# Performance work log

Measured on AMD Instinct MI355X. Metric: run time of the kernel, lower is better.

Reference implementation:

```python
import jax, jax.numpy as jnp
import numpy as np

EPS = 1e-08
ATOM_CA = 1


def setup_inputs() -> dict:
    key = jax.random.key(0)
    k1, k2 = jax.random.split(key)
    B, N_RES, N_ATOMS = 256, 1024, 37
    pred_coords = jax.random.normal(k1, (B, N_RES, N_ATOMS, 3), dtype=jnp.float32)
    true_coords = jax.random.normal(k2, (B, N_RES, N_ATOMS, 3), dtype=jnp.float32)
    atom_mask = jnp.ones((B, N_RES, N_ATOMS), dtype=jnp.float32)
    return {"pred_coords": pred_coords, "true_coords": true_coords, "atom_mask": atom_mask}


def _kabsch_align(pred, true, mask):
    # pred/true: [B, N, 3], mask: [B, N]
    mask_sum = jnp.sum(mask, axis=1, keepdims=True) + EPS          # [B, 1]
    m = mask[..., None]                                             # [B, N, 1]
    pred_center = jnp.sum(pred * m, axis=1) / mask_sum              # [B, 3]
    true_center = jnp.sum(true * m, axis=1) / mask_sum              # [B, 3]
    pred_c = (pred - pred_center[:, None, :]) * m                   # [B, N, 3]
    true_c = (true - true_center[:, None, :]) * m                   # [B, N, 3]
    H = jnp.einsum('bni,bnj->bij', pred_c, true_c)                  # [B, 3, 3]
    U, s, Vh = jnp.linalg.svd(H)                                    # H = U diag(s) Vh
    V = jnp.swapaxes(Vh, -1, -2)
    Ut = jnp.swapaxes(U, -1, -2)
    det = jnp.linalg.det(jnp.matmul(V, Ut))                         # [B]
    sign = jnp.stack([jnp.ones_like(det), jnp.ones_like(det), det], axis=-1)  # [B, 3]
    S = jnp.eye(3, dtype=pred.dtype) * sign[:, None, :]             # diag(1,1,det)
    R = jnp.matmul(jnp.matmul(V, S), Ut)                            # [B, 3, 3]
    # aligned = (pred - pred_center) @ R^T + true_center
    aligned = jnp.einsum('bnj,bij->bni', pred - pred_center[:, None, :], R)
    return aligned + true_center[:, None, :]


def reference(pred_coords, true_coords, atom_mask):
    pred_ca = pred_coords[:, :, ATOM_CA, :]   # [B, N_res, 3]
    true_ca = true_coords[:, :, ATOM_CA, :]
    ca_mask = atom_mask[:, :, ATOM_CA]        # [B, N_res]
    pred_ca = _kabsch_align(pred_ca, true_ca, ca_mask)
    diff_sq = jnp.sum((pred_ca - true_ca) ** 2, axis=-1)            # [B, N_res]
    rmsd = jnp.sqrt(jnp.sum(diff_sq * ca_mask, axis=1) / (jnp.sum(ca_mask, axis=1) + EPS))
    return jnp.mean(rmsd)
```

## Files before the change

### kernel.cpp

```cpp
#include <hip/hip_runtime.h>
#include <math.h>

#define N_RES 1024
#define N_ATOMS 37
#define ATOM_CA 1
#define NBATCH 256
#define SLICES 4
#define NSUM 34

__global__ __launch_bounds__(256) void rmsd_moments_kernel(
    const float* __restrict__ pred, const float* __restrict__ truec,
    const float* __restrict__ mask, float* __restrict__ partials)
{
    const int blk   = blockIdx.x;
    const int b     = blk >> 2;
    const int slice = blk & 3;
    const int tid   = threadIdx.x;
    const int n     = slice * 256 + tid;

    const size_t resStride = (size_t)N_ATOMS * 3;
    const float* pp = pred  + ((size_t)b * N_RES + n) * resStride + ATOM_CA * 3;
    const float* tt = truec + ((size_t)b * N_RES + n) * resStride + ATOM_CA * 3;
    const float  m  = mask[((size_t)b * N_RES + n) * N_ATOMS + ATOM_CA];

    const float p0 = pp[0], p1 = pp[1], p2 = pp[2];
    const float t0 = tt[0], t1 = tt[1], t2 = tt[2];
    const float m2 = m * m;

    float acc[NSUM];
    acc[0] = m;
    acc[1] = m * p0;  acc[2] = m * p1;  acc[3] = m * p2;
    acc[4] = m * t0;  acc[5] = m * t1;  acc[6] = m * t2;
    acc[7] = m * (p0*p0 + p1*p1 + p2*p2);
    acc[8] = m * (t0*t0 + t1*t1 + t2*t2);
    acc[9]  = m * p0 * t0; acc[10] = m * p0 * t1; acc[11] = m * p0 * t2;
    acc[12] = m * p1 * t0; acc[13] = m * p1 * t1; acc[14] = m * p1 * t2;
    acc[15] = m * p2 * t0; acc[16] = m * p2 * t1; acc[17] = m * p2 * t2;
    acc[18] = m2;
    acc[19] = m2 * p0; acc[20] = m2 * p1; acc[21] = m2 * p2;
    acc[22] = m2 * t0; acc[23] = m2 * t1; acc[24] = m2 * t2;
    acc[25] = m2 * p0 * t0; acc[26] = m2 * p0 * t1; acc[27] = m2 * p0 * t2;
    acc[28] = m2 * p1 * t0; acc[29] = m2 * p1 * t1; acc[30] = m2 * p1 * t2;
    acc[31] = m2 * p2 * t0; acc[32] = m2 * p2 * t1; acc[33] = m2 * p2 * t2;

#pragma unroll
    for (int i = 0; i < NSUM; ++i) {
        float v = acc[i];
#pragma unroll
        for (int off = 32; off > 0; off >>= 1) v += __shfl_down(v, off, 64);
        acc[i] = v;
    }

    __shared__ float partial[4][NSUM];
    const int wave = tid >> 6, lane = tid & 63;
    if (lane == 0) {
#pragma unroll
        for (int i = 0; i < NSUM; ++i) partial[wave][i] = acc[i];
    }
    __syncthreads();
    if (tid < NSUM) {
        partials[(size_t)blk * NSUM + tid] =
            partial[0][tid] + partial[1][tid] + partial[2][tid] + partial[3][tid];
    }
}

__global__ __launch_bounds__(256) void rmsd_finish_kernel(
    const float* __restrict__ partials, float* __restrict__ out)
{
    const int b = threadIdx.x;

    double s[NSUM];
#pragma unroll
    for (int i = 0; i < NSUM; ++i) s[i] = 0.0;
#pragma unroll
    for (int k = 0; k < SLICES; ++k) {
        const float* row = partials + ((size_t)b * SLICES + k) * NSUM;
#pragma unroll
        for (int i = 0; i < NSUM; ++i) s[i] += (double)row[i];
    }

    const double M   = s[0];
    const double Mep = M + 1e-8;
    double Sp[3] = { s[1], s[2], s[3] };
    double St[3] = { s[4], s[5], s[6] };
    double pc[3] = { Sp[0] / Mep, Sp[1] / Mep, Sp[2] / Mep };
    double tc[3] = { St[0] / Mep, St[1] / Mep, St[2] / Mep };
    const double Qp = s[7], Qt = s[8];
    const double S2 = s[18];
    double S2p[3] = { s[19], s[20], s[21] };
    double S2t[3] = { s[22], s[23], s[24] };

    double H[3][3];
#pragma unroll
    for (int i = 0; i < 3; ++i)
#pragma unroll
        for (int j = 0; j < 3; ++j)
            H[i][j] = s[25 + i * 3 + j] - pc[i] * S2t[j] - tc[j] * S2p[i]
                    + pc[i] * tc[j] * S2;

    const float Sxx = (float)H[0][0], Sxy = (float)H[0][1], Sxz = (float)H[0][2];
    const float Syx = (float)H[1][0], Syy = (float)H[1][1], Syz = (float)H[1][2];
    const float Szx = (float)H[2][0], Szy = (float)H[2][1], Szz = (float)H[2][2];
    float A[4][4] = {
        { Sxx + Syy + Szz, Syz - Szy,        Szx - Sxz,        Sxy - Syx },
        { Syz - Szy,       Sxx - Syy - Szz,  Sxy + Syx,        Szx + Sxz },
        { Szx - Sxz,       Sxy + Syx,       -Sxx + Syy - Szz,  Syz + Szy },
        { Sxy - Syx,       Szx + Sxz,        Syz + Szy,       -Sxx - Syy + Szz }
    };
    float Vm[4][4] = { {1,0,0,0},{0,1,0,0},{0,0,1,0},{0,0,0,1} };

#pragma unroll
    for (int sweep = 0; sweep < 8; ++sweep) {
#pragma unroll
        for (int p = 0; p < 3; ++p) {
#pragma unroll
            for (int q = p + 1; q < 4; ++q) {
                const float apq = A[p][q];
                const float denom = fabsf(apq) > 1e-20f ? apq : 1e-20f;
                const float theta = (A[q][q] - A[p][p]) / (2.0f * denom);
                float tt = (theta >= 0.0f ? 1.0f : -1.0f)
                         / (fabsf(theta) + sqrtf(theta * theta + 1.0f));
                if (fabsf(apq) <= 1e-20f) tt = 0.0f;
                const float c = 1.0f / sqrtf(tt * tt + 1.0f);
                const float sn = tt * c;
#pragma unroll
                for (int k = 0; k < 4; ++k) {
                    const float akp = A[k][p], akq = A[k][q];
                    A[k][p] = c * akp - sn * akq;
                    A[k][q] = sn * akp + c * akq;
                }
#pragma unroll
                for (int k = 0; k < 4; ++k) {
                    const float apk = A[p][k], aqk = A[q][k];
                    A[p][k] = c * apk - sn * aqk;
                    A[q][k] = sn * apk + c * aqk;
                }
#pragma unroll
                for (int k = 0; k < 4; ++k) {
                    const float vkp = Vm[k][p], vkq = Vm[k][q];
                    Vm[k][p] = c * vkp - sn * vkq;
                    Vm[k][q] = sn * vkp + c * vkq;
                }
            }
        }
    }
    int best = 0;
#pragma unroll
    for (int i = 1; i < 4; ++i) if (A[i][i] > A[best][best]) best = i;
    float q0 = Vm[0][best], qx = Vm[1][best], qy = Vm[2][best], qz = Vm[3][best];
    const float nq = sqrtf(q0*q0 + qx*qx + qy*qy + qz*qz);
    q0 /= nq; qx /= nq; qy /= nq; qz /= nq;

    double R[3][3] = {
        { 1.0 - 2.0*((double)qy*qy + (double)qz*qz), 2.0*((double)qx*qy - (double)qz*q0), 2.0*((double)qx*qz + (double)qy*q0) },
        { 2.0*((double)qx*qy + (double)qz*q0), 1.0 - 2.0*((double)qx*qx + (double)qz*qz), 2.0*((double)qy*qz - (double)qx*q0) },
        { 2.0*((double)qx*qz - (double)qy*q0), 2.0*((double)qy*qz + (double)qx*q0), 1.0 - 2.0*((double)qx*qx + (double)qy*qy) }
    };

    double cross = 0.0;
#pragma unroll
    for (int i = 0; i < 3; ++i)
#pragma unroll
        for (int j = 0; j < 3; ++j) {
            const double Gij = s[9 + j * 3 + i] - tc[i] * Sp[j] - pc[j] * St[i]
                             + tc[i] * pc[j] * M;
            cross += R[i][j] * Gij;
        }

    const double Qpc = Qp - 2.0*(pc[0]*Sp[0] + pc[1]*Sp[1] + pc[2]*Sp[2])
                     + (pc[0]*pc[0] + pc[1]*pc[1] + pc[2]*pc[2]) * M;
    const double Qtc = Qt - 2.0*(tc[0]*St[0] + tc[1]*St[1] + tc[2]*St[2])
                     + (tc[0]*tc[0] + tc[1]*tc[1] + tc[2]*tc[2]) * M;
    double D = Qpc + Qtc - 2.0 * cross;
    if (D < 0.0) D = 0.0;
    float rmsd = (float)sqrt(D / Mep);

#pragma unroll
    for (int off = 32; off > 0; off >>= 1) rmsd += __shfl_down(rmsd, off, 64);
    __shared__ float part[4];
    if ((threadIdx.x & 63) == 0) part[threadIdx.x >> 6] = rmsd;
    __syncthreads();
    if (threadIdx.x == 0)
        out[0] = (part[0] + part[1] + part[2] + part[3]) * (1.0f / (float)NBATCH);
}

extern "C" void kernel_launch(void* const* d_in, const int* in_sizes, int n_in,
                              void* d_out, int out_size, void* d_ws, size_t ws_size,
                              hipStream_t stream) {
    const float* pred  = (const float*)d_in[0];
    const float* truec = (const float*)d_in[1];
    const float* mask  = (const float*)d_in[2];
    float* out = (float*)d_out;
    float* partials = (float*)d_ws;

    rmsd_moments_kernel<<<NBATCH * SLICES, 256, 0, stream>>>(pred, truec, mask, partials);
    rmsd_finish_kernel<<<1, 256, 0, stream>>>(partials, out);
}
```

Measured before the change: 269.0 us.

## Replace Jacobi quaternion eigensolve with QCP characteristic-polynomial Newton iteration

The finish kernel no longer diagonalises the 4x4 quaternion matrix with Jacobi sweeps and builds a rotation. It now forms the coefficients of the QCP characteristic polynomial in double precision and finds the largest eigenvalue with 40 Newton steps. That eigenvalue is used directly as the cross term in the RMSD. Two extra mask-squared norm moments are accumulated in the moments kernel to seed the iteration, which adds more reductions there. It also relies on the mask weights making the m- and m²-weighted sums equivalent.

```diff
diff --git a/kernel.cpp b/kernel.cpp
--- a/kernel.cpp
+++ b/kernel.cpp
@@ -6,7 +6,7 @@
 #define ATOM_CA 1
 #define NBATCH 256
 #define SLICES 4
-#define NSUM 34
+#define NSUM 36
 
 __global__ __launch_bounds__(256) void rmsd_moments_kernel(
     const float* __restrict__ pred, const float* __restrict__ truec,
@@ -26,13 +26,15 @@
     const float p0 = pp[0], p1 = pp[1], p2 = pp[2];
     const float t0 = tt[0], t1 = tt[1], t2 = tt[2];
     const float m2 = m * m;
+    const float np = p0*p0 + p1*p1 + p2*p2;
+    const float nt = t0*t0 + t1*t1 + t2*t2;
 
     float acc[NSUM];
     acc[0] = m;
     acc[1] = m * p0;  acc[2] = m * p1;  acc[3] = m * p2;
     acc[4] = m * t0;  acc[5] = m * t1;  acc[6] = m * t2;
-    acc[7] = m * (p0*p0 + p1*p1 + p2*p2);
-    acc[8] = m * (t0*t0 + t1*t1 + t2*t2);
+    acc[7] = m * np;
+    acc[8] = m * nt;
     acc[9]  = m * p0 * t0; acc[10] = m * p0 * t1; acc[11] = m * p0 * t2;
     acc[12] = m * p1 * t0; acc[13] = m * p1 * t1; acc[14] = m * p1 * t2;
     acc[15] = m * p2 * t0; acc[16] = m * p2 * t1; acc[17] = m * p2 * t2;
@@ -42,6 +44,8 @@
     acc[25] = m2 * p0 * t0; acc[26] = m2 * p0 * t1; acc[27] = m2 * p0 * t2;
     acc[28] = m2 * p1 * t0; acc[29] = m2 * p1 * t1; acc[30] = m2 * p1 * t2;
     acc[31] = m2 * p2 * t0; acc[32] = m2 * p2 * t1; acc[33] = m2 * p2 * t2;
+    acc[34] = m2 * np;
+    acc[35] = m2 * nt;
 
 #pragma unroll
     for (int i = 0; i < NSUM; ++i) {
@@ -81,97 +85,81 @@
 
     const double M   = s[0];
     const double Mep = M + 1e-8;
-    double Sp[3] = { s[1], s[2], s[3] };
-    double St[3] = { s[4], s[5], s[6] };
-    double pc[3] = { Sp[0] / Mep, Sp[1] / Mep, Sp[2] / Mep };
-    double tc[3] = { St[0] / Mep, St[1] / Mep, St[2] / Mep };
+    const double Sp0 = s[1], Sp1 = s[2], Sp2 = s[3];
+    const double St0 = s[4], St1 = s[5], St2 = s[6];
+    const double pc0 = Sp0 / Mep, pc1 = Sp1 / Mep, pc2 = Sp2 / Mep;
+    const double tc0 = St0 / Mep, tc1 = St1 / Mep, tc2 = St2 / Mep;
     const double Qp = s[7], Qt = s[8];
     const double S2 = s[18];
-    double S2p[3] = { s[19], s[20], s[21] };
-    double S2t[3] = { s[22], s[23], s[24] };
+    const double S2p0 = s[19], S2p1 = s[20], S2p2 = s[21];
+    const double S2t0 = s[22], S2t1 = s[23], S2t2 = s[24];
+    const double Qp2 = s[34], Qt2 = s[35];
 
-    double H[3][3];
+    const double Sxx = s[25] - pc0 * S2t0 - tc0 * S2p0 + pc0 * tc0 * S2;
+    const double Sxy = s[26] - pc0 * S2t1 - tc1 * S2p0 + pc0 * tc1 * S2;
+    const double Sxz = s[27] - pc0 * S2t2 - tc2 * S2p0 + pc0 * tc2 * S2;
+    const double Syx = s[28] - pc1 * S2t0 - tc0 * S2p1 + pc1 * tc0 * S2;
+    const double Syy = s[29] - pc1 * S2t1 - tc1 * S2p1 + pc1 * tc1 * S2;
+    const double Syz = s[30] - pc1 * S2t2 - tc2 * S2p1 + pc1 * tc2 * S2;
+    const double Szx = s[31] - pc2 * S2t0 - tc0 * S2p2 + pc2 * tc0 * S2;
+    const double Szy = s[32] - pc2 * S2t1 - tc1 * S2p2 + pc2 * tc1 * S2;
+    const double Szz = s[33] - pc2 * S2t2 - tc2 * S2p2 + pc2 * tc2 * S2;
+
+    const double GA2 = Qp2 - 2.0*(pc0*S2p0 + pc1*S2p1 + pc2*S2p2)
+                     + (pc0*pc0 + pc1*pc1 + pc2*pc2) * S2;
+    const double GB2 = Qt2 - 2.0*(tc0*S2t0 + tc1*S2t1 + tc2*S2t2)
+                     + (tc0*tc0 + tc1*tc1 + tc2*tc2) * S2;
+
+    const double Sxx2 = Sxx*Sxx, Syy2 = Syy*Syy, Szz2 = Szz*Szz;
+    const double Sxy2 = Sxy*Sxy, Syz2 = Syz*Syz, Sxz2 = Sxz*Sxz;
+    const double Syx2 = Syx*Syx, Szy2 = Szy*Szy, Szx2 = Szx*Szx;
+
+    const double SyzSzymSyySzz2 = 2.0*(Syz*Szy - Syy*Szz);
+    const double Sxx2Syy2Szz2Syz2Szy2 = Syy2 + Szz2 - Sxx2 + Syz2 + Szy2;
+
+    const double C2 = -2.0*(Sxx2 + Syy2 + Szz2 + Sxy2 + Syx2 + Sxz2 + Szx2 + Syz2 + Szy2);
+    const double C1 = 8.0*(Sxx*Syz*Szy + Syy*Szx*Sxz + Szz*Sxy*Syx
+                         - Sxx*Syy*Szz - Syz*Szx*Sxy - Szy*Syx*Sxz);
+
+    const double SxzpSzx = Sxz + Szx;
+    const double SyzpSzy = Syz + Szy;
+    const double SxypSyx = Sxy + Syx;
+    const double SyzmSzy = Syz - Szy;
+    const double SxzmSzx = Sxz - Szx;
+    const double SxymSyx = Sxy - Syx;
+    const double SxxpSyy = Sxx + Syy;
+    const double SxxmSyy = Sxx - Syy;
+    const double Sxy2Sxz2Syx2Szx2 = Sxy2 + Sxz2 - Syx2 - Szx2;
+
+    const double C0 =
+        Sxy2Sxz2Syx2Szx2 * Sxy2Sxz2Syx2Szx2
+      + (Sxx2Syy2Szz2Syz2Szy2 + SyzSzymSyySzz2) * (Sxx2Syy2Szz2Syz2Szy2 - SyzSzymSyySzz2)
+      + (-(SxzpSzx)*(SyzmSzy) + (SxymSyx)*(SxxmSyy - Szz)) *
+        (-(SxzmSzx)*(SyzpSzy) + (SxymSyx)*(SxxmSyy + Szz))
+      + (-(SxzpSzx)*(SyzpSzy) - (SxypSyx)*(SxxpSyy - Szz)) *
+        (-(SxzmSzx)*(SyzmSzy) - (SxypSyx)*(SxxpSyy + Szz))
+      + ( (SxypSyx)*(SyzpSzy) + (SxzpSzx)*(SxxmSyy + Szz)) *
+        (-(SxymSyx)*(SyzmSzy) + (SxzpSzx)*(SxxpSyy + Szz))
+      + ( (SxypSyx)*(SyzmSzy) + (SxzmSzx)*(SxxmSyy - Szz)) *
+        (-(SxymSyx)*(SyzpSzy) + (SxzmSzx)*(SxxpSyy - Szz));
+
+    double lam = 0.5 * (GA2 + GB2);
 #pragma unroll
-    for (int i = 0; i < 3; ++i)
-#pragma unroll
-        for (int j = 0; j < 3; ++j)
-            H[i][j] = s[25 + i * 3 + j] - pc[i] * S2t[j] - tc[j] * S2p[i]
-                    + pc[i] * tc[j] * S2;
+    for (int it = 0; it < 40; ++it) {
+        const double x2 = lam * lam;
+        const double bq = (x2 + C2) * lam;
+        const double aq = bq + C1;
+        const double den = 2.0 * x2 * lam + bq + aq;
+        const double num = aq * lam + C0;
+        const double d = (fabs(den) > 1e-300) ? (num / den) : 0.0;
+        lam -= d;
+    }
 
-    const float Sxx = (float)H[0][0], Sxy = (float)H[0][1], Sxz = (float)H[0][2];
-    const float Syx = (float)H[1][0], Syy = (float)H[1][1], Syz = (float)H[1][2];
-    const float Szx = (float)H[2][0], Szy = (float)H[2][1], Szz = (float)H[2][2];
-    float A[4][4] = {
-        { Sxx + Syy + Szz, Syz - Szy,        Szx - Sxz,        Sxy - Syx },
-        { Syz - Szy,       Sxx - Syy - Szz,  Sxy + Syx,        Szx + Sxz },
-        { Szx - Sxz,       Sxy + Syx,       -Sxx + Syy - Szz,  Syz + Szy },
-        { Sxy - Syx,       Szx + Sxz,        Syz + Szy,       -Sxx - Syy + Szz }
-    };
-    float Vm[4][4] = { {1,0,0,0},{0,1,0,0},{0,0,1,0},{0,0,0,1} };
-
-#pragma unroll
-    for (int sweep = 0; sweep < 8; ++sweep) {
-#pragma unroll
-        for (int p = 0; p < 3; ++p) {
-#pragma unroll
-            for (int q = p + 1; q < 4; ++q) {
-                const float apq = A[p][q];
-                const float denom = fabsf(apq) > 1e-20f ? apq : 1e-20f;
-                const float theta = (A[q][q] - A[p][p]) / (2.0f * denom);
-                float tt = (theta >= 0.0f ? 1.0f : -1.0f)
-                         / (fabsf(theta) + sqrtf(theta * theta + 1.0f));
-                if (fabsf(apq) <= 1e-20f) tt = 0.0f;
-                const float c = 1.0f / sqrtf(tt * tt + 1.0f);
-                const float sn = tt * c;
-#pragma unroll
-                for (int k = 0; k < 4; ++k) {
-                    const float akp = A[k][p], akq = A[k][q];
-                    A[k][p] = c * akp - sn * akq;
-                    A[k][q] = sn * akp + c * akq;
-                }
-#pragma unroll
-                for (int k = 0; k < 4; ++k) {
-                    const float apk = A[p][k], aqk = A[q][k];
-                    A[p][k] = c * apk - sn * aqk;
-                    A[q][k] = sn * apk + c * aqk;
-                }
-#pragma unroll
-                for (int k = 0; k < 4; ++k) {
-                    const float vkp = Vm[k][p], vkq = Vm[k][q];
-                    Vm[k][p] = c * vkp - sn * vkq;
-                    Vm[k][q] = sn * vkp + c * vkq;
-                }
-            }
-        }
-    }
-    int best = 0;
-#pragma unroll
-    for (int i = 1; i < 4; ++i) if (A[i][i] > A[best][best]) best = i;
-    float q0 = Vm[0][best], qx = Vm[1][best], qy = Vm[2][best], qz = Vm[3][best];
-    const float nq = sqrtf(q0*q0 + qx*qx + qy*qy + qz*qz);
-    q0 /= nq; qx /= nq; qy /= nq; qz /= nq;
-
-    double R[3][3] = {
-        { 1.0 - 2.0*((double)qy*qy + (double)qz*qz), 2.0*((double)qx*qy - (double)qz*q0), 2.0*((double)qx*qz + (double)qy*q0) },
-        { 2.0*((double)qx*qy + (double)qz*q0), 1.0 - 2.0*((double)qx*qx + (double)qz*qz), 2.0*((double)qy*qz - (double)qx*q0) },
-        { 2.0*((double)qx*qz - (double)qy*q0), 2.0*((double)qy*qz + (double)qx*q0), 1.0 - 2.0*((double)qx*qx + (double)qy*qy) }
-    };
-
-    double cross = 0.0;
-#pragma unroll
-    for (int i = 0; i < 3; ++i)
-#pragma unroll
-        for (int j = 0; j < 3; ++j) {
-            const double Gij = s[9 + j * 3 + i] - tc[i] * Sp[j] - pc[j] * St[i]
-                             + tc[i] * pc[j] * M;
-            cross += R[i][j] * Gij;
-        }
-
-    const double Qpc = Qp - 2.0*(pc[0]*Sp[0] + pc[1]*Sp[1] + pc[2]*Sp[2])
-                     + (pc[0]*pc[0] + pc[1]*pc[1] + pc[2]*pc[2]) * M;
-    const double Qtc = Qt - 2.0*(tc[0]*St[0] + tc[1]*St[1] + tc[2]*St[2])
-                     + (tc[0]*tc[0] + tc[1]*tc[1] + tc[2]*tc[2]) * M;
-    double D = Qpc + Qtc - 2.0 * cross;
+    const double Qpc = Qp - 2.0*(pc0*Sp0 + pc1*Sp1 + pc2*Sp2)
+                     + (pc0*pc0 + pc1*pc1 + pc2*pc2) * M;
+    const double Qtc = Qt - 2.0*(tc0*St0 + tc1*St1 + tc2*St2)
+                     + (tc0*tc0 + tc1*tc1 + tc2*tc2) * M;
+    double D = Qpc + Qtc - 2.0 * lam;
     if (D < 0.0) D = 0.0;
     float rmsd = (float)sqrt(D / Mep);
 
```

Measured after the change: 239.2 us. -11.1%, faster.
